# Optimization experiments

Measured on AMD Instinct MI355X. Metric: run time of the kernel, lower is better.

The kernel has to match this reference:

```python
import jax, jax.numpy as jnp
import numpy as np
from jax import lax

H = 256  # hidden_size


def _conv1d(x, w, b):
    # x: (N, Cin, L), w: (Cout, Cin, K) -> (N, Cout, L-K+1), VALID, stride 1
    y = lax.conv_general_dilated(x, w, window_strides=(1,), padding='VALID',
                                 dimension_numbers=('NCH', 'OIH', 'NCH'))
    return y + b[None, :, None]


def _gru_dir(x, Wih, Whh, bih, bhh):
    # x: (L, N, H). Torch GRU cell equations.
    L, N, _ = x.shape
    gi = jnp.einsum('lnh,gh->lng', x, Wih) + bih  # (L, N, 3H) precomputed input gates
    h0 = jnp.zeros((N, H), x.dtype)

    def step(h, gi_t):
        gh = h @ Whh.T + bhh                       # (N, 3H)
        ir, iz, inn = jnp.split(gi_t, 3, axis=-1)
        hr, hz, hn = jnp.split(gh, 3, axis=-1)
        r = jax.nn.sigmoid(ir + hr)
        z = jax.nn.sigmoid(iz + hz)
        n = jnp.tanh(inn + r * hn)
        h_new = (1.0 - z) * n + z * h
        return h_new, h_new

    hT, ys = lax.scan(step, h0, gi)
    return ys, hT  # (L, N, H), (N, H)


def setup_inputs() -> dict:
    key = jax.random.key(0)
    ks = jax.random.split(key, 14)
    N, C, L = 32, 13, 4096
    s = 0.1
    inp = {
        'X': jax.random.normal(ks[0], (N, C, L), jnp.float32),
        'W1': jax.random.normal(ks[1], (H // 2, C, 3), jnp.float32) * s,
        'b1': jax.random.normal(ks[2], (H // 2,), jnp.float32) * s,
        'W2': jax.random.normal(ks[3], (H, H // 2, 3), jnp.float32) * s,
        'b2': jax.random.normal(ks[4], (H,), jnp.float32) * s,
        'Wih_f': jax.random.normal(ks[5], (3 * H, H), jnp.float32) * s,
        'Whh_f': jax.random.normal(ks[6], (3 * H, H), jnp.float32) * s,
        'bih_f': jax.random.normal(ks[7], (3 * H,), jnp.float32) * s,
        'bhh_f': jax.random.normal(ks[8], (3 * H,), jnp.float32) * s,
        'Wih_b': jax.random.normal(ks[9], (3 * H, H), jnp.float32) * s,
        'Whh_b': jax.random.normal(ks[10], (3 * H, H), jnp.float32) * s,
        'bih_b': jax.random.normal(ks[11], (3 * H,), jnp.float32) * s,
        'bhh_b': jax.random.normal(ks[12], (3 * H,), jnp.float32) * s,
    }
    return inp


def reference(X, W1, b1, W2, b2, Wih_f, Whh_f, bih_f, bhh_f,
              Wih_b, Whh_b, bih_b, bhh_b):
    # dropouts are identity in eval mode; N>1 so squeeze() is a no-op
    x = _conv1d(X, W1, b1)           # (N, H/2, L-2)
    x = _conv1d(x, W2, b2)           # (N, H,   L-4)
    x = x[:, :, ::2]                 # MaxPool1d(kernel=1, stride=2) == stride-2 subsample
    x = jnp.transpose(x, (2, 0, 1))  # (L', N, H)

    out_f, hT_f = _gru_dir(x, Wih_f, Whh_f, bih_f, bhh_f)
    # backward direction: reverse time, scan, reverse outputs
    out_b_rev, hT_b = _gru_dir(x[::-1], Wih_b, Whh_b, bih_b, bhh_b)
    out_b = out_b_rev[::-1]

    # original: fwd + flip(bwd along FEATURE axis), averaged, ReLU (faithful to np.flip(axis=-1))
    comb = jax.nn.relu((out_f + out_b[:, :, ::-1]) * 0.5)  # (L', N, H)
    hidden_last = hT_b[None]                                # hidden[-1].unsqueeze(0): (1, N, H)
    return comb, hidden_last
```

## Files before the change

### kernel.cpp

```cpp
#include <hip/hip_runtime.h>
#include <hip/hip_fp16.h>
#include <cstdint>
#include <cstddef>

#define L_SEQ 2046
#define NBATCH 32
#define HID 256
#define M_PAD 65536

typedef _Float16 h2vec __attribute__((ext_vector_type(2)));

static __device__ __forceinline__ uint32_t pack2(float a, float b) {
  __half2 h = __floats2half2_rn(a, b);
  return __builtin_bit_cast(uint32_t, h);
}

static __device__ __forceinline__ float fdot2u(uint32_t w, uint32_t h, float c) {
#if __has_builtin(__builtin_amdgcn_fdot2)
  return __builtin_amdgcn_fdot2(__builtin_bit_cast(h2vec, w),
                                __builtin_bit_cast(h2vec, h), c, false);
#else
  __half2 a = __builtin_bit_cast(__half2, w);
  __half2 b = __builtin_bit_cast(__half2, h);
  float2 fa = __half22float2(a), fb = __half22float2(b);
  return c + fa.x * fb.x + fa.y * fb.y;
#endif
}

__global__ void k_conv_im2col(const float* __restrict__ X,
                              const float* __restrict__ W1,
                              const float* __restrict__ b1,
                              __half* __restrict__ A1h) {
  int j   = threadIdx.x;
  int row = blockIdx.x;
  int l2 = row >> 5, n = row & 31;
  float v = 0.f;
  if (l2 < L_SEQ) {
    int ci = j / 3;
    int k  = j - 3 * ci;
    int p  = 2 * l2 + k;
    const float* xb = X + (size_t)n * 13 * 4096 + p;
    const float* w  = W1 + ci * 39;
    float acc = b1[ci];
#pragma unroll
    for (int c = 0; c < 13; c++) {
      const float* xp = xb + (size_t)c * 4096;
      acc += xp[0] * w[3*c+0] + xp[1] * w[3*c+1] + xp[2] * w[3*c+2];
    }
    v = acc;
  }
  A1h[(size_t)row * 384 + j] = __float2half(v);
}

__global__ __launch_bounds__(256, 4) void k_gemm_h(
    const __half* __restrict__ A, const float* __restrict__ B,
    const float* __restrict__ bias, __half* __restrict__ C,
    int K, int ldC, int col_off) {
  __shared__ float As[32][132];
  __shared__ float Bs[32][132];
  const int tid = threadIdx.x;
  const int m_blk = blockIdx.x * 128;
  const int n_blk = blockIdx.y * 128;
  const int tx = tid & 15, ty = tid >> 4;
  const int m0 = tx * 8, n0 = ty * 8;
  const int sr = tid >> 3;
  const int sc = 4 * (tid & 7);
  const int ar = tid >> 1;
  const int ak = 16 * (tid & 1);

  float acc[8][8];
#pragma unroll
  for (int i = 0; i < 8; i++)
#pragma unroll
    for (int j = 0; j < 8; j++) acc[i][j] = 0.f;

  for (int kc = 0; kc < K; kc += 32) {
    const __half* ap = A + (size_t)(m_blk + ar) * K + kc + ak;
    uint4 h0 = *(const uint4*)(ap);
    uint4 h1 = *(const uint4*)(ap + 8);
    {
      uint32_t hw[8] = {h0.x, h0.y, h0.z, h0.w, h1.x, h1.y, h1.z, h1.w};
#pragma unroll
      for (int p = 0; p < 8; p++) {
        float2 f = __half22float2(__builtin_bit_cast(__half2, hw[p]));
        As[ak + 2*p    ][ar] = f.x;
        As[ak + 2*p + 1][ar] = f.y;
      }
    }
#pragma unroll
    for (int i = 0; i < 4; i++) {
      int r = i * 32 + sr;
      float4 vb = *(const float4*)(B + (size_t)(n_blk + r) * K + kc + sc);
      Bs[sc+0][r] = vb.x; Bs[sc+1][r] = vb.y; Bs[sc+2][r] = vb.z; Bs[sc+3][r] = vb.w;
    }
    __syncthreads();
#pragma unroll 8
    for (int k = 0; k < 32; k++) {
      float a[8], b[8];
      *(float4*)(a)     = *(const float4*)&As[k][m0];
      *(float4*)(a + 4) = *(const float4*)&As[k][m0 + 4];
      *(float4*)(b)     = *(const float4*)&Bs[k][n0];
      *(float4*)(b + 4) = *(const float4*)&Bs[k][n0 + 4];
#pragma unroll
      for (int i = 0; i < 8; i++)
#pragma unroll
        for (int j = 0; j < 8; j++) acc[i][j] += a[i] * b[j];
    }
    __syncthreads();
  }
  float bj[8];
#pragma unroll
  for (int j = 0; j < 8; j++) bj[j] = bias[n_blk + n0 + j];
#pragma unroll
  for (int i = 0; i < 8; i++) {
    uint4 o;
    o.x = pack2(acc[i][0] + bj[0], acc[i][1] + bj[1]);
    o.y = pack2(acc[i][2] + bj[2], acc[i][3] + bj[3]);
    o.z = pack2(acc[i][4] + bj[4], acc[i][5] + bj[5]);
    o.w = pack2(acc[i][6] + bj[6], acc[i][7] + bj[7]);
    *(uint4*)(C + (size_t)(m_blk + m0 + i) * ldC + col_off + n_blk + n0) = o;
  }
}

__global__ void k_packw(const float* __restrict__ Whh_f,
                        const float* __restrict__ Whh_b,
                        uint4* __restrict__ Wpk) {
  int idx = blockIdx.x * 256 + threadIdx.x;
  int d   = idx / 24576;
  int r   = idx - d * 24576;
  int jq  = r >> 9;
  int tid = r & 511;
  int q   = jq / 3, gt = jq - 3 * q;
  int lane = tid & 63, wave = tid >> 6;
  int kh = lane & 1, g = wave * 32 + (lane >> 1);
  const float* W = d ? Whh_b : Whh_f;
  const float* src = W + (size_t)(gt * 256 + g) * 256 + kh * 128 + 8 * q;
  uint4 o;
  o.x = pack2(src[0], src[1]);
  o.y = pack2(src[2], src[3]);
  o.z = pack2(src[4], src[5]);
  o.w = pack2(src[6], src[7]);
  Wpk[(size_t)idx] = o;
}

__global__ __attribute__((amdgpu_flat_work_group_size(512, 512),
                          amdgpu_waves_per_eu(2, 2)))
void k_gru(
    const __half* __restrict__ gih, const uint4* __restrict__ Wpk,
    const float* __restrict__ bhh_f, const float* __restrict__ bhh_b,
    float* __restrict__ outF, __half* __restrict__ outBh,
    float* __restrict__ hT) {
  const int blk = blockIdx.x;
  const int dir = blk >> 5;
  const int n   = blk & 31;
  const int tid = threadIdx.x;
  const int lane = tid & 63;
  const int kh  = lane & 1;
  const int g   = (tid >> 6) * 32 + (lane >> 1);

  const float* bhh = dir ? bhh_b : bhh_f;

  uint4 wv[48];
  {
    const uint4* wp = Wpk + (size_t)dir * 24576 + tid;
#pragma unroll
    for (int j = 0; j < 48; j++) wv[j] = wp[j * 512];
#pragma unroll
    for (int j = 0; j < 48; j++) {
      asm volatile("" : "+v"(wv[j].x), "+v"(wv[j].y), "+v"(wv[j].z), "+v"(wv[j].w));
    }
  }
  const float bh0 = bhh[g];
  const float bh1 = bhh[256 + g];
  const float bh2 = bhh[512 + g];

  __shared__ __align__(16) __half hs[2][256];
  if (tid < 128) ((uint32_t*)hs)[tid] = 0u;
  float hp = 0.f;

  const __half* gr = gih + ((size_t)(dir ? (size_t)(L_SEQ - 1) * NBATCH : 0) + n) * 1536
                         + dir * 768 + g;
  const ptrdiff_t gstep = dir ? -(ptrdiff_t)(NBATCH * 1536) : (ptrdiff_t)(NBATCH * 1536);
  __half pi0 = __float2half(0.f), pi1 = pi0, pi2 = pi0;
  if (kh == 0) { pi0 = gr[0]; pi1 = gr[256]; pi2 = gr[512]; }
  __syncthreads();

  for (int t = 0; t < L_SEQ; t++) {
    const uint4* hb = (const uint4*)hs[t & 1];
    float a0 = 0.f, a1 = 0.f, a2 = 0.f;
#pragma unroll
    for (int q = 0; q < 16; q++) {
      uint4 hq = hb[q * 2 + kh];
      uint4 u0 = wv[q * 3 + 0];
      uint4 u1 = wv[q * 3 + 1];
      uint4 u2 = wv[q * 3 + 2];
      a0 = fdot2u(u0.x, hq.x, a0);
      a0 = fdot2u(u0.y, hq.y, a0);
      a0 = fdot2u(u0.z, hq.z, a0);
      a0 = fdot2u(u0.w, hq.w, a0);
      a1 = fdot2u(u1.x, hq.x, a1);
      a1 = fdot2u(u1.y, hq.y, a1);
      a1 = fdot2u(u1.z, hq.z, a1);
      a1 = fdot2u(u1.w, hq.w, a1);
      a2 = fdot2u(u2.x, hq.x, a2);
      a2 = fdot2u(u2.y, hq.y, a2);
      a2 = fdot2u(u2.z, hq.z, a2);
      a2 = fdot2u(u2.w, hq.w, a2);
    }
    a0 += __shfl_xor(a0, 1);
    a1 += __shfl_xor(a1, 1);
    a2 += __shfl_xor(a2, 1);

    if (kh == 0) {
      float hr = a0 + bh0;
      float hz = a1 + bh1;
      float hn = a2 + bh2;
      float ir  = __half2float(pi0);
      float iz  = __half2float(pi1);
      float inn = __half2float(pi2);
      float rr = 1.f / (1.f + __expf(-(ir + hr)));
      float zz = 1.f / (1.f + __expf(-(iz + hz)));
      float e  = __expf(2.f * (inn + rr * hn));
      float nn = 1.f - 2.f / (e + 1.f);
      float hnew = (1.f - zz) * nn + zz * hp;
      hp = hnew;
      __half hh = __float2half(hnew);
      int swi = ((g & 127) >> 3) * 16 + (g >> 7) * 8 + (g & 7);
      hs[(t + 1) & 1][swi] = hh;
      const int l = dir ? (L_SEQ - 1 - t) : t;
      uint32_t oi = ((uint32_t)l * NBATCH + n) * HID + g;
      if (dir == 0) outF[oi] = hnew;
      else          outBh[oi] = hh;
      gr += gstep;
      if (t + 1 < L_SEQ) { pi0 = gr[0]; pi1 = gr[256]; pi2 = gr[512]; }
    }
    __syncthreads();
  }
  if (dir == 1 && kh == 0) hT[n * HID + g] = hp;
}

__global__ void k_combine(float* __restrict__ outF,
                          const __half* __restrict__ outBh) {
  int idx = blockIdx.x * 256 + threadIdx.x;
  int c = idx & 255;
  float v = 0.5f * (outF[idx] + __half2float(outBh[idx + 255 - 2 * c]));
  outF[idx] = v > 0.f ? v : 0.f;
}

extern "C" void kernel_launch(void* const* d_in, const int* in_sizes, int n_in,
                              void* d_out, int out_size, void* d_ws, size_t ws_size,
                              hipStream_t stream) {
  const float* X     = (const float*)d_in[0];
  const float* W1    = (const float*)d_in[1];
  const float* b1    = (const float*)d_in[2];
  const float* W2    = (const float*)d_in[3];
  const float* b2    = (const float*)d_in[4];
  const float* Wih_f = (const float*)d_in[5];
  const float* Whh_f = (const float*)d_in[6];
  const float* bih_f = (const float*)d_in[7];
  const float* bhh_f = (const float*)d_in[8];
  const float* Wih_b = (const float*)d_in[9];
  const float* Whh_b = (const float*)d_in[10];
  const float* bih_b = (const float*)d_in[11];
  const float* bhh_b = (const float*)d_in[12];

  char* wsb = (char*)d_ws;
  __half* gih   = (__half*)(wsb);
  __half* A1h   = (__half*)(wsb + 201326592);
  __half* outBh = (__half*)(wsb + 201326592);
  uint4*  Wpk   = (uint4*)(wsb + 234848768);

  float*  outF  = (float*)d_out;
  __half* xsubh = (__half*)d_out;
  float*  hT    = outF + (size_t)L_SEQ * NBATCH * HID;

  k_conv_im2col<<<dim3(M_PAD), 384, 0, stream>>>(X, W1, b1, A1h);
  k_gemm_h<<<dim3(512, 2), 256, 0, stream>>>(A1h, W2, b2, xsubh, 384, 256, 0);
  k_packw<<<dim3(192), 256, 0, stream>>>(Whh_f, Whh_b, Wpk);
  k_gemm_h<<<dim3(512, 6), 256, 0, stream>>>(xsubh, Wih_f, bih_f, gih, 256, 1536, 0);
  k_gemm_h<<<dim3(512, 6), 256, 0, stream>>>(xsubh, Wih_b, bih_b, gih, 256, 1536, 768);
  k_gru<<<dim3(64), 512, 0, stream>>>(gih, Wpk, bhh_f, bhh_b, outF, outBh, hT);
  k_combine<<<dim3(65472), 256, 0, stream>>>(outF, outBh);
}
```

Before: 3.753 ms.

## Compute GRU recurrent matvec with MFMA 16x16x32 instead of fdot2

The per-step hidden-to-hidden matvec now uses MFMA f16 instructions. The hidden vector is broadcast across all 16 B columns, and the weights are repacked into the MFMA A-operand layout. Results are staged through a shared-memory array with an extra barrier, and the gate math moves to the first 256 threads. This cuts the VALU dot-product instruction count per step, but wastes 15/16 of the MFMA columns and adds a sync and an LDS round trip per timestep.

```diff
diff --git a/kernel.cpp b/kernel.cpp
--- a/kernel.cpp
+++ b/kernel.cpp
@@ -9,22 +9,12 @@
 #define M_PAD 65536
 
 typedef _Float16 h2vec __attribute__((ext_vector_type(2)));
+typedef _Float16 half8 __attribute__((ext_vector_type(8)));
+typedef float f32x4 __attribute__((ext_vector_type(4)));
 
 static __device__ __forceinline__ uint32_t pack2(float a, float b) {
   __half2 h = __floats2half2_rn(a, b);
   return __builtin_bit_cast(uint32_t, h);
-}
-
-static __device__ __forceinline__ float fdot2u(uint32_t w, uint32_t h, float c) {
-#if __has_builtin(__builtin_amdgcn_fdot2)
-  return __builtin_amdgcn_fdot2(__builtin_bit_cast(h2vec, w),
-                                __builtin_bit_cast(h2vec, h), c, false);
-#else
-  __half2 a = __builtin_bit_cast(__half2, w);
-  __half2 b = __builtin_bit_cast(__half2, h);
-  float2 fa = __half22float2(a), fb = __half22float2(b);
-  return c + fa.x * fb.x + fa.y * fb.y;
-#endif
 }
 
 __global__ void k_conv_im2col(const float* __restrict__ X,
@@ -127,14 +117,15 @@
                         uint4* __restrict__ Wpk) {
   int idx = blockIdx.x * 256 + threadIdx.x;
   int d   = idx / 24576;
-  int r   = idx - d * 24576;
-  int jq  = r >> 9;
-  int tid = r & 511;
-  int q   = jq / 3, gt = jq - 3 * q;
-  int lane = tid & 63, wave = tid >> 6;
-  int kh = lane & 1, g = wave * 32 + (lane >> 1);
+  int r2  = idx - d * 24576;
+  int tl  = r2 >> 9;
+  int tid = r2 & 511;
+  int w = tid >> 6, lane = tid & 63;
+  int group = tl >> 3, kc = tl & 7;
+  int row = w * 96 + group * 16 + (lane & 15);
+  int kb  = kc * 32 + (lane >> 4) * 8;
   const float* W = d ? Whh_b : Whh_f;
-  const float* src = W + (size_t)(gt * 256 + g) * 256 + kh * 128 + 8 * q;
+  const float* src = W + (size_t)row * 256 + kb;
   uint4 o;
   o.x = pack2(src[0], src[1]);
   o.y = pack2(src[2], src[3]);
@@ -155,10 +146,8 @@
   const int n   = blk & 31;
   const int tid = threadIdx.x;
   const int lane = tid & 63;
-  const int kh  = lane & 1;
-  const int g   = (tid >> 6) * 32 + (lane >> 1);
-
-  const float* bhh = dir ? bhh_b : bhh_f;
+  const int w    = tid >> 6;
+  const int g    = tid;
 
   uint4 wv[48];
   {
@@ -170,11 +159,12 @@
       asm volatile("" : "+v"(wv[j].x), "+v"(wv[j].y), "+v"(wv[j].z), "+v"(wv[j].w));
     }
   }
-  const float bh0 = bhh[g];
-  const float bh1 = bhh[256 + g];
-  const float bh2 = bhh[512 + g];
+  const float* bhh = dir ? bhh_b : bhh_f;
+  float bh0 = 0.f, bh1 = 0.f, bh2 = 0.f;
+  if (tid < 256) { bh0 = bhh[g]; bh1 = bhh[256 + g]; bh2 = bhh[512 + g]; }
 
   __shared__ __align__(16) __half hs[2][256];
+  __shared__ __align__(16) float  pa[768];
   if (tid < 128) ((uint32_t*)hs)[tid] = 0u;
   float hp = 0.f;
 
@@ -182,39 +172,40 @@
                          + dir * 768 + g;
   const ptrdiff_t gstep = dir ? -(ptrdiff_t)(NBATCH * 1536) : (ptrdiff_t)(NBATCH * 1536);
   __half pi0 = __float2half(0.f), pi1 = pi0, pi2 = pi0;
-  if (kh == 0) { pi0 = gr[0]; pi1 = gr[256]; pi2 = gr[512]; }
+  if (tid < 256) { pi0 = gr[0]; pi1 = gr[256]; pi2 = gr[512]; }
+
+  const int qoff = (lane >> 4) << 4;
+  const int rowb = w * 96 + (lane >> 4) * 4;
   __syncthreads();
 
   for (int t = 0; t < L_SEQ; t++) {
-    const uint4* hb = (const uint4*)hs[t & 1];
-    float a0 = 0.f, a1 = 0.f, a2 = 0.f;
-#pragma unroll
-    for (int q = 0; q < 16; q++) {
-      uint4 hq = hb[q * 2 + kh];
-      uint4 u0 = wv[q * 3 + 0];
-      uint4 u1 = wv[q * 3 + 1];
-      uint4 u2 = wv[q * 3 + 2];
-      a0 = fdot2u(u0.x, hq.x, a0);
-      a0 = fdot2u(u0.y, hq.y, a0);
-      a0 = fdot2u(u0.z, hq.z, a0);
-      a0 = fdot2u(u0.w, hq.w, a0);
-      a1 = fdot2u(u1.x, hq.x, a1);
-      a1 = fdot2u(u1.y, hq.y, a1);
-      a1 = fdot2u(u1.z, hq.z, a1);
-      a1 = fdot2u(u1.w, hq.w, a1);
-      a2 = fdot2u(u2.x, hq.x, a2);
-      a2 = fdot2u(u2.y, hq.y, a2);
-      a2 = fdot2u(u2.z, hq.z, a2);
-      a2 = fdot2u(u2.w, hq.w, a2);
-    }
-    a0 += __shfl_xor(a0, 1);
-    a1 += __shfl_xor(a1, 1);
-    a2 += __shfl_xor(a2, 1);
-
-    if (kh == 0) {
-      float hr = a0 + bh0;
-      float hz = a1 + bh1;
-      float hn = a2 + bh2;
+    const char* hcur = (const char*)hs[t & 1];
+    half8 bf[8];
+#pragma unroll
+    for (int kc = 0; kc < 8; kc++)
+      bf[kc] = __builtin_bit_cast(half8, *(const uint4*)(hcur + kc * 64 + qoff));
+
+    f32x4 acc[6];
+#pragma unroll
+    for (int g6 = 0; g6 < 6; g6++) acc[g6] = (f32x4){0.f, 0.f, 0.f, 0.f};
+#pragma unroll
+    for (int kc = 0; kc < 8; kc++)
+#pragma unroll
+      for (int g6 = 0; g6 < 6; g6++)
+        acc[g6] = __builtin_amdgcn_mfma_f32_16x16x32_f16(
+            __builtin_bit_cast(half8, wv[g6 * 8 + kc]), bf[kc], acc[g6], 0, 0, 0);
+
+    if ((lane & 15) == 0) {
+#pragma unroll
+      for (int g6 = 0; g6 < 6; g6++)
+        *(f32x4*)&pa[rowb + g6 * 16] = acc[g6];
+    }
+    __syncthreads();
+
+    if (tid < 256) {
+      float hr = pa[g]       + bh0;
+      float hz = pa[256 + g] + bh1;
+      float hn = pa[512 + g] + bh2;
       float ir  = __half2float(pi0);
       float iz  = __half2float(pi1);
       float inn = __half2float(pi2);
@@ -225,8 +216,7 @@
       float hnew = (1.f - zz) * nn + zz * hp;
       hp = hnew;
       __half hh = __float2half(hnew);
-      int swi = ((g & 127) >> 3) * 16 + (g >> 7) * 8 + (g & 7);
-      hs[(t + 1) & 1][swi] = hh;
+      hs[(t + 1) & 1][g] = hh;
       const int l = dir ? (L_SEQ - 1 - t) : t;
       uint32_t oi = ((uint32_t)l * NBATCH + n) * HID + g;
       if (dir == 0) outF[oi] = hnew;
@@ -236,7 +226,7 @@
     }
     __syncthreads();
   }
-  if (dir == 1 && kh == 0) hT[n * HID + g] = hp;
+  if (dir == 1 && tid < 256) hT[n * HID + g] = hp;
 }
 
 __global__ void k_combine(float* __restrict__ outF,
```

New measurement: 3.778 ms. About the same (+0.7%).
